# Kernel optimization log

Hardware: AMD Instinct MI355X
Metric: run time of the kernel (lower is better)

The kernel has to match this reference:

```python
import jax, jax.numpy as jnp
import numpy as np

B, C_IN, C_OUT, N, K = 32, 128, 128, 128, 3


def setup_inputs() -> dict:
    key = jax.random.key(0)
    k1, k2 = jax.random.split(key)
    # input image batch [B, C_in, N, N]
    x = jax.random.normal(k1, (B, C_IN, N, N), dtype=jnp.float32)
    # learned kernel, matches torch.rand init: [C_out, C_in, K, K]
    kernel = jax.random.uniform(k2, (C_OUT, C_IN, K, K), dtype=jnp.float32)
    return {"x": x, "kernel": kernel}


def reference(x, kernel):
    # BlockConv's banded block-sparse BCSR matmul is mathematically a
    # SAME-zero-padded 2D cross-correlation (no kernel flip):
    #   out[b,o,i,p] = sum_{c,k,d} kernel[o,c,k,d] * x[b,c,i+k-K//2,p+d-K//2]
    # (border blocks in _apply_constraint truncate the kernel exactly like
    #  zero padding). bias=False, so no bias term.
    return jax.lax.conv_general_dilated(
        x, kernel,
        window_strides=(1, 1),
        padding="SAME",
        dimension_numbers=("NCHW", "OIHW", "NCHW"),
    )
```

## Files before the change

### kernel.cpp

```cpp
#include <hip/hip_runtime.h>
#include <hip/hip_bf16.h>

#define B_    32
#define CIN   128
#define COUT  128
#define NN    128
#define PPAD  130
#define ROWE  (PPAD * CIN)

#define JCOLS 66
#define CHROW (JCOLS * 16)
#define CH5   (4 * CHROW)

typedef __attribute__((ext_vector_type(8))) short short8;
typedef __attribute__((ext_vector_type(4))) float float4v;

static __device__ inline unsigned short f2bf(float f) {
    union { float f; unsigned u; } v; v.f = f;
    unsigned u = v.u;
    unsigned r = u + 0x7FFFu + ((u >> 16) & 1u);
    return (unsigned short)(r >> 16);
}

static __device__ inline void gll16(const unsigned short* g, unsigned short* l) {
    __builtin_amdgcn_global_load_lds((const __attribute__((address_space(1))) unsigned int*)g,
                                     (__attribute__((address_space(3))) unsigned int*)l,
                                     16, 0, 0);
}

__global__ __launch_bounds__(256) void xpose_kernel(const float* __restrict__ x,
                                                    unsigned short* __restrict__ xT) {
    int b = blockIdx.x >> 7;
    int i = blockIdx.x & 127;
    __shared__ unsigned short tile[CIN * PPAD];
    int tid = threadIdx.x;
    const float* src = x + ((size_t)(b * CIN) * NN + i) * NN;
    #pragma unroll
    for (int e = 0; e < 64; ++e) {
        int idx = e * 256 + tid;
        int c = idx >> 7;
        int p = idx & 127;
        tile[c * PPAD + p] = f2bf(src[(size_t)c * (NN * NN) + p]);
    }
    __syncthreads();
    unsigned short* dst = xT + (size_t)(b * NN + i) * ROWE;
    #pragma unroll
    for (int e = 0; e < 32; ++e) {
        int pi = e * 256 + tid;
        int c2 = (pi & 63) * 2;
        int p  = pi >> 6;
        ushort2 v;
        v.x = tile[c2 * PPAD + p];
        v.y = tile[(c2 + 1) * PPAD + p];
        int pp = p + 1;
        int sl = (c2 >> 3) ^ (pp & 15);
        *(ushort2*)(dst + (size_t)pp * CIN + sl * 8 + (c2 & 7)) = v;
    }
    if (tid < 128) {
        dst[tid] = 0;
        dst[(size_t)129 * CIN + tid] = 0;
    }
}

__global__ __launch_bounds__(256) void ktrans_kernel(const float* __restrict__ kern,
                                                     unsigned short* __restrict__ kT2) {
    int idx = blockIdx.x * 256 + threadIdx.x;
    if (idx >= COUT * CIN * 9) return;
    int c  = idx & 127;
    int o  = (idx >> 7) & 127;
    int kd = idx >> 14;
    int k = kd / 3, d = kd % 3;
    float v = kern[(((size_t)o * CIN + c) * 3 + k) * 3 + d];
    kT2[((size_t)(kd * 16 + (c >> 3)) * 128 + o) * 8 + (c & 7)] = f2bf(v);
}

__global__ __launch_bounds__(512, 4) void conv_mfma6_kernel(const unsigned short* __restrict__ xT,
                                                            const unsigned short* __restrict__ kT2,
                                                            float* __restrict__ out) {
    __shared__ unsigned short xs[CH5 * 8];

    int wg = blockIdx.x;
    int lb = (wg & 7) * 512 + (wg >> 3);
    int b  = lb >> 7;
    int t  = lb & 127;
    int ph = t >> 6;
    int rp = t & 63;
    const int pb0 = ph * 64;

    int tid  = threadIdx.x;
    int lane = tid & 63;
    int wave = tid >> 6;
    int wo = wave >> 2;
    int wr = (wave >> 1) & 1;
    int wp = wave & 1;
    int ob  = wo * 64;
    int l15 = lane & 15;
    int lg  = lane >> 4;

    {
        const unsigned short* xrow_base = xT + (size_t)b * NN * ROWE;
        #pragma unroll
        for (int s = 0; s < 9; ++s) {
            int W = s * 512 + tid;
            if (W < CH5) {
                int r    = W / CHROW;
                int rem  = W - r * CHROW;
                int grow = rp * 2 - 1 + r;
                int growc = grow < 0 ? 0 : (grow > NN - 1 ? NN - 1 : grow);
                const unsigned short* src = xrow_base + (size_t)growc * ROWE
                                          + ((size_t)pb0 + (rem >> 4)) * CIN
                                          + (rem & 15) * 8;
                gll16(src, xs + (size_t)W * 8);
            }
        }
    }
    __syncthreads();

    if (rp == 0) {
        for (int W = tid; W < CHROW; W += 512)
            *(short8*)(xs + (size_t)W * 8) = (short8)(0);
    }
    if (rp == 63) {
        for (int W = 3 * CHROW + tid; W < 4 * CHROW; W += 512)
            *(short8*)(xs + (size_t)W * 8) = (short8)(0);
    }
    if (rp == 0 || rp == 63) __syncthreads();

    float4v acc[4][2];
    #pragma unroll
    for (int m = 0; m < 4; ++m) {
        acc[m][0] = (float4v)(0.0f);
        acc[m][1] = (float4v)(0.0f);
    }

    #pragma unroll
    for (int kd = 0; kd < 9; ++kd) {
        const int k = kd / 3, d = kd % 3;
        const unsigned short* srow = xs + (size_t)(wr + k) * CHROW * 8;
        #pragma unroll
        for (int cc = 0; cc < 4; ++cc) {
            const int cslot = cc * 4 + lg;
            short8 a[4], bt[2];
            #pragma unroll
            for (int m = 0; m < 4; ++m)
                a[m] = *(const short8*)(kT2 +
                    ((size_t)((kd * 16 + cslot) * 128) + ob + m * 16 + l15) * 8);
            int j0 = wp * 32 + l15 + d;
            int j1 = j0 + 16;
            bt[0] = *(const short8*)(srow + ((size_t)j0 * 16 + (cslot ^ (j0 & 15))) * 8);
            bt[1] = *(const short8*)(srow + ((size_t)j1 * 16 + (cslot ^ (j1 & 15))) * 8);
            #pragma unroll
            for (int m = 0; m < 4; ++m) {
                acc[m][0] = __builtin_amdgcn_mfma_f32_16x16x32_bf16(a[m], bt[0], acc[m][0], 0, 0, 0);
                acc[m][1] = __builtin_amdgcn_mfma_f32_16x16x32_bf16(a[m], bt[1], acc[m][1], 0, 0, 0);
            }
        }
    }

    int row = rp * 2 + wr;
    float* op = out + (size_t)b * COUT * NN * NN + (size_t)row * NN;
    #pragma unroll
    for (int m = 0; m < 4; ++m) {
        #pragma unroll
        for (int n = 0; n < 2; ++n) {
            int p = pb0 + wp * 32 + n * 16 + l15;
            #pragma unroll
            for (int r = 0; r < 4; ++r) {
                int o = ob + m * 16 + lg * 4 + r;
                op[(size_t)o * (NN * NN) + p] = acc[m][n][r];
            }
        }
    }
}

__global__ __launch_bounds__(256) void conv_naive_kernel(const float* __restrict__ x,
                                                         const float* __restrict__ kern,
                                                         float* __restrict__ out) {
    size_t idx = (size_t)blockIdx.x * 256 + threadIdx.x;
    int p = idx & 127;
    size_t t = idx >> 7;
    int i = t & 127; t >>= 7;
    int o = t & 127;
    int b = (int)(t >> 7);
    float s = 0.f;
    for (int c = 0; c < CIN; ++c) {
        #pragma unroll
        for (int k = 0; k < 3; ++k) {
            int r = i + k - 1;
            if (r < 0 || r >= NN) continue;
            #pragma unroll
            for (int d = 0; d < 3; ++d) {
                int q = p + d - 1;
                if (q < 0 || q >= NN) continue;
                s += kern[(((size_t)o * CIN + c) * 3 + k) * 3 + d]
                   * x[(((size_t)b * CIN + c) * NN + r) * NN + q];
            }
        }
    }
    out[idx] = s;
}

extern "C" void kernel_launch(void* const* d_in, const int* in_sizes, int n_in,
                              void* d_out, int out_size, void* d_ws, size_t ws_size,
                              hipStream_t stream) {
    const float* x    = (const float*)d_in[0];
    const float* kern = (const float*)d_in[1];
    float* out = (float*)d_out;

    const size_t xT_bytes  = (size_t)B_ * NN * ROWE * 2;
    const size_t kT_bytes  = (size_t)9 * 16 * 128 * 8 * 2;

    if (ws_size >= xT_bytes + kT_bytes) {
        unsigned short* xT  = (unsigned short*)d_ws;
        unsigned short* kT2 = (unsigned short*)((char*)d_ws + xT_bytes);
        hipLaunchKernelGGL(xpose_kernel, dim3(B_ * NN), dim3(256), 0, stream, x, xT);
        hipLaunchKernelGGL(ktrans_kernel, dim3(576), dim3(256), 0, stream, kern, kT2);
        hipLaunchKernelGGL(conv_mfma6_kernel, dim3(4096), dim3(512), 0, stream, xT, kT2, out);
    } else {
        hipLaunchKernelGGL(conv_naive_kernel, dim3(67108864 / 256), dim3(256), 0, stream,
                           x, kern, out);
    }
}
```

Measured before the change: 283.9 us.

## Widen conv workgroup tile to full 128-column rows, doubling per-wave output tile

Each workgroup now covers full image rows (all 128 columns plus padding) instead of a 64-column half, so the halo columns are no longer loaded twice and the grid is halved. Each wave computes a 64x64 output tile with 16 accumulators, so every weight fragment loaded from global memory feeds twice as many MFMAs. In exchange, LDS per workgroup grows to about 130 KB and register use rises, so launch bounds drop to 2 and occupancy falls.

After: 290.6 us. +2.4%, slower.

```diff
diff --git a/kernel.cpp b/kernel.cpp
--- a/kernel.cpp
+++ b/kernel.cpp
@@ -7,10 +7,8 @@
 #define NN    128
 #define PPAD  130
 #define ROWE  (PPAD * CIN)
-
-#define JCOLS 66
-#define CHROW (JCOLS * 16)
-#define CH5   (4 * CHROW)
+#define CHROW7 (PPAD * 16)
+#define CH7    (4 * CHROW7)
 
 typedef __attribute__((ext_vector_type(8))) short short8;
 typedef __attribute__((ext_vector_type(4))) float float4v;
@@ -74,86 +72,83 @@
     kT2[((size_t)(kd * 16 + (c >> 3)) * 128 + o) * 8 + (c & 7)] = f2bf(v);
 }
 
-__global__ __launch_bounds__(512, 4) void conv_mfma6_kernel(const unsigned short* __restrict__ xT,
+__global__ __launch_bounds__(512, 2) void conv_mfma7_kernel(const unsigned short* __restrict__ xT,
                                                             const unsigned short* __restrict__ kT2,
                                                             float* __restrict__ out) {
-    __shared__ unsigned short xs[CH5 * 8];
+    __shared__ unsigned short xs[4 * ROWE];
 
     int wg = blockIdx.x;
-    int lb = (wg & 7) * 512 + (wg >> 3);
-    int b  = lb >> 7;
-    int t  = lb & 127;
-    int ph = t >> 6;
-    int rp = t & 63;
-    const int pb0 = ph * 64;
+    int lb = (wg & 7) * 256 + (wg >> 3);
+    int b  = lb >> 6;
+    int rp = lb & 63;
 
     int tid  = threadIdx.x;
     int lane = tid & 63;
     int wave = tid >> 6;
     int wo = wave >> 2;
     int wr = (wave >> 1) & 1;
-    int wp = wave & 1;
+    int wq = wave & 1;
     int ob  = wo * 64;
+    int pb  = wq * 64;
     int l15 = lane & 15;
     int lg  = lane >> 4;
 
     {
         const unsigned short* xrow_base = xT + (size_t)b * NN * ROWE;
         #pragma unroll
-        for (int s = 0; s < 9; ++s) {
+        for (int s = 0; s < 17; ++s) {
             int W = s * 512 + tid;
-            if (W < CH5) {
-                int r    = W / CHROW;
-                int rem  = W - r * CHROW;
+            if (W < CH7) {
+                int r    = W / CHROW7;
+                int rem  = W - r * CHROW7;
                 int grow = rp * 2 - 1 + r;
                 int growc = grow < 0 ? 0 : (grow > NN - 1 ? NN - 1 : grow);
-                const unsigned short* src = xrow_base + (size_t)growc * ROWE
-                                          + ((size_t)pb0 + (rem >> 4)) * CIN
-                                          + (rem & 15) * 8;
-                gll16(src, xs + (size_t)W * 8);
+                gll16(xrow_base + (size_t)growc * ROWE + (size_t)rem * 8,
+                      xs + (size_t)W * 8);
             }
         }
     }
     __syncthreads();
 
     if (rp == 0) {
-        for (int W = tid; W < CHROW; W += 512)
+        for (int W = tid; W < CHROW7; W += 512)
             *(short8*)(xs + (size_t)W * 8) = (short8)(0);
     }
     if (rp == 63) {
-        for (int W = 3 * CHROW + tid; W < 4 * CHROW; W += 512)
+        for (int W = 3 * CHROW7 + tid; W < 4 * CHROW7; W += 512)
             *(short8*)(xs + (size_t)W * 8) = (short8)(0);
     }
     if (rp == 0 || rp == 63) __syncthreads();
 
-    float4v acc[4][2];
-    #pragma unroll
-    for (int m = 0; m < 4; ++m) {
-        acc[m][0] = (float4v)(0.0f);
-        acc[m][1] = (float4v)(0.0f);
-    }
+    float4v acc[4][4];
+    #pragma unroll
+    for (int m = 0; m < 4; ++m)
+        #pragma unroll
+        for (int n = 0; n < 4; ++n)
+            acc[m][n] = (float4v)(0.0f);
 
     #pragma unroll
     for (int kd = 0; kd < 9; ++kd) {
         const int k = kd / 3, d = kd % 3;
-        const unsigned short* srow = xs + (size_t)(wr + k) * CHROW * 8;
+        const unsigned short* srow = xs + (size_t)(wr + k) * ROWE;
         #pragma unroll
         for (int cc = 0; cc < 4; ++cc) {
             const int cslot = cc * 4 + lg;
-            short8 a[4], bt[2];
+            short8 a[4], bt[4];
             #pragma unroll
             for (int m = 0; m < 4; ++m)
                 a[m] = *(const short8*)(kT2 +
                     ((size_t)((kd * 16 + cslot) * 128) + ob + m * 16 + l15) * 8);
-            int j0 = wp * 32 + l15 + d;
-            int j1 = j0 + 16;
-            bt[0] = *(const short8*)(srow + ((size_t)j0 * 16 + (cslot ^ (j0 & 15))) * 8);
-            bt[1] = *(const short8*)(srow + ((size_t)j1 * 16 + (cslot ^ (j1 & 15))) * 8);
-            #pragma unroll
-            for (int m = 0; m < 4; ++m) {
-                acc[m][0] = __builtin_amdgcn_mfma_f32_16x16x32_bf16(a[m], bt[0], acc[m][0], 0, 0, 0);
-                acc[m][1] = __builtin_amdgcn_mfma_f32_16x16x32_bf16(a[m], bt[1], acc[m][1], 0, 0, 0);
-            }
+            #pragma unroll
+            for (int n = 0; n < 4; ++n) {
+                int pp = pb + n * 16 + l15 + d;
+                bt[n] = *(const short8*)(srow + ((size_t)pp * 16 + (cslot ^ (pp & 15))) * 8);
+            }
+            #pragma unroll
+            for (int m = 0; m < 4; ++m)
+                #pragma unroll
+                for (int n = 0; n < 4; ++n)
+                    acc[m][n] = __builtin_amdgcn_mfma_f32_16x16x32_bf16(a[m], bt[n], acc[m][n], 0, 0, 0);
         }
     }
 
@@ -162,8 +157,8 @@
     #pragma unroll
     for (int m = 0; m < 4; ++m) {
         #pragma unroll
-        for (int n = 0; n < 2; ++n) {
-            int p = pb0 + wp * 32 + n * 16 + l15;
+        for (int n = 0; n < 4; ++n) {
+            int p = pb + n * 16 + l15;
             #pragma unroll
             for (int r = 0; r < 4; ++r) {
                 int o = ob + m * 16 + lg * 4 + r;
@@ -215,7 +210,7 @@
         unsigned short* kT2 = (unsigned short*)((char*)d_ws + xT_bytes);
         hipLaunchKernelGGL(xpose_kernel, dim3(B_ * NN), dim3(256), 0, stream, x, xT);
         hipLaunchKernelGGL(ktrans_kernel, dim3(576), dim3(256), 0, stream, kern, kT2);
-        hipLaunchKernelGGL(conv_mfma6_kernel, dim3(4096), dim3(512), 0, stream, xT, kT2, out);
+        hipLaunchKernelGGL(conv_mfma7_kernel, dim3(2048), dim3(512), 0, stream, xT, kT2, out);
     } else {
         hipLaunchKernelGGL(conv_naive_kernel, dim3(67108864 / 256), dim3(256), 0, stream,
                            x, kern, out);
```
